# Optimization experiments

Hardware: AMD Instinct MI355X
Metric: run time of the kernel (lower is better)

## Reference

```python
import jax, jax.numpy as jnp
import numpy as np

N = 100000
E = 800000
D_IN = 64
D_HID = 64
D_OUT = 47


def gcn_conv(x, edge_index, W, b):
    # GCNConv with normalize=False: linear transform then sum-aggregate over edges.
    h = x @ W                              # [N, d_out]
    src, dst = edge_index[0], edge_index[1]
    msg = h[src]                           # [E, d_out] gather
    agg = jax.ops.segment_sum(msg, dst, num_segments=N)  # [N, d_out] scatter-add
    return agg + b


def setup_inputs() -> dict:
    key = jax.random.key(0)
    ks = jax.random.split(key, 8)
    x = jax.random.normal(ks[0], (N, D_IN), dtype=jnp.float32)
    edge_index = jax.random.randint(ks[1], (2, E), 0, N, dtype=jnp.int64)
    # Glorot-ish init for weights, zeros for bias (as in GCNConv.reset_parameters)
    def glorot(k, fan_in, fan_out):
        s = jnp.sqrt(6.0 / (fan_in + fan_out))
        return jax.random.uniform(k, (fan_in, fan_out), jnp.float32, -s, s)
    W1 = glorot(ks[2], D_IN, D_HID)
    b1 = jnp.zeros((D_HID,), jnp.float32)
    W2 = glorot(ks[3], D_HID, D_HID)
    b2 = jnp.zeros((D_HID,), jnp.float32)
    W3 = glorot(ks[4], D_HID, D_OUT)
    b3 = jnp.zeros((D_OUT,), jnp.float32)
    return {"x": x, "edge_index": edge_index,
            "W1": W1, "b1": b1, "W2": W2, "b2": b2, "W3": W3, "b3": b3}


def reference(x, edge_index, W1, b1, W2, b2, W3, b3):
    # Layer 1: conv -> relu (dropout is identity at inference)
    h = jax.nn.relu(gcn_conv(x, edge_index, W1, b1))
    # Layer 2
    h = jax.nn.relu(gcn_conv(h, edge_index, W2, b2))
    # Output layer + log_softmax over classes
    out = gcn_conv(h, edge_index, W3, b3)
    return jax.nn.log_softmax(out, axis=-1)
```

## Files before the change

kernel.cpp:

```cpp
#include <hip/hip_runtime.h>
#include <cmath>


#define B1_EPB 4096
#define BKT_SH 8
#define CHUNK  256
#define PSTRIDE 512

typedef __attribute__((ext_vector_type(8))) short bf8;
typedef __attribute__((ext_vector_type(4))) float f4;

__device__ __forceinline__ unsigned int f2bf(float x) {
  unsigned int u = __float_as_uint(x);
  return (u + 0x7FFFu + ((u >> 16) & 1u)) >> 16;
}
__device__ __forceinline__ float bflo(unsigned int u) { return __uint_as_float(u << 16); }
__device__ __forceinline__ float bfhi(unsigned int u) { return __uint_as_float(u & 0xFFFF0000u); }

__global__ void bhist_cvt_k(const int* __restrict__ dsti, int* __restrict__ part,
                            int ne, const float* __restrict__ x,
                            unsigned short* __restrict__ xb, int n4,
                            int nbkt, int nseg) {
  __shared__ int lh[PSTRIDE];
  const int b = blockIdx.x, t = threadIdx.x;
  if (b < nseg) {
    for (int i = t; i < PSTRIDE; i += 256) lh[i] = 0;
    __syncthreads();
    const int base = b * B1_EPB;
    const int m = min(B1_EPB, ne - base);
    for (int i = t; i < m; i += 256) atomicAdd(&lh[dsti[base + i] >> BKT_SH], 1);
    __syncthreads();
    for (int i = t; i < PSTRIDE; i += 256) part[b * PSTRIDE + i] = lh[i];
  }
  const int gid = b * 256 + t, gst = gridDim.x * 256;
  for (int j = gid; j < n4; j += gst) {
    float4 v = ((const float4*)x)[j];
    ushort4 o;
    o.x = (unsigned short)f2bf(v.x); o.y = (unsigned short)f2bf(v.y);
    o.z = (unsigned short)f2bf(v.z); o.w = (unsigned short)f2bf(v.w);
    ((ushort4*)xb)[j] = o;
  }
}

__global__ void bscan_k(const int* __restrict__ part, int* __restrict__ bbase,
                        int* __restrict__ bcur, int nbkt, int nseg, int ne) {
  __shared__ int sh[512];
  const int t = threadIdx.x;
  int s0 = 0, s1 = 0, s2 = 0, s3 = 0, s4 = 0, s5 = 0, s6 = 0, s7 = 0;
  int b = 0;
  for (; b + 7 < nseg; b += 8) {
    s0 += part[(b + 0) * PSTRIDE + t];
    s1 += part[(b + 1) * PSTRIDE + t];
    s2 += part[(b + 2) * PSTRIDE + t];
    s3 += part[(b + 3) * PSTRIDE + t];
    s4 += part[(b + 4) * PSTRIDE + t];
    s5 += part[(b + 5) * PSTRIDE + t];
    s6 += part[(b + 6) * PSTRIDE + t];
    s7 += part[(b + 7) * PSTRIDE + t];
  }
  for (; b < nseg; ++b) s0 += part[b * PSTRIDE + t];
  const int s = ((s0 + s1) + (s2 + s3)) + ((s4 + s5) + (s6 + s7));
  sh[t] = s; __syncthreads();
  for (int o = 1; o < 512; o <<= 1) {
    int v = (t >= o) ? sh[t - o] : 0; __syncthreads();
    sh[t] += v; __syncthreads();
  }
  if (t < nbkt) { int e = sh[t] - s; bbase[t] = e; bcur[t] = e; }
  if (t == 0) bbase[nbkt] = ne;
}

__global__ void bucket_k(const int* __restrict__ srci, const int* __restrict__ dsti,
                         int* __restrict__ bcur, uint2* __restrict__ ebuf,
                         int ne, int nbkt) {
  __shared__ int lhist[512], lbase[512];
  const int t = threadIdx.x;
  const int base = blockIdx.x * B1_EPB;
  const int m = min(B1_EPB, ne - base);
  for (int i = t; i < nbkt; i += 256) lhist[i] = 0;
  __syncthreads();
  for (int i = t; i < m; i += 256) atomicAdd(&lhist[dsti[base + i] >> BKT_SH], 1);
  __syncthreads();
  for (int i = t; i < nbkt; i += 256) {
    int c = lhist[i];
    lbase[i] = c ? atomicAdd(&bcur[i], c) : 0;
  }
  __syncthreads();
  for (int i = t; i < nbkt; i += 256) lhist[i] = 0;
  __syncthreads();
  for (int i = t; i < m; i += 256) {
    const int s = srci[base + i], d = dsti[base + i];
    const int b = d >> BKT_SH;
    const int p = lbase[b] + atomicAdd(&lhist[b], 1);
    ebuf[p] = make_uint2((unsigned)s, (unsigned)d);
  }
}

__global__ void fillb_k(const uint2* __restrict__ ebuf, const int* __restrict__ bbase,
                        int* __restrict__ row_off, int* __restrict__ ssrc,
                        int n, int ne) {
  __shared__ int lcnt[256], lpre[256], lcur[256];
  const int b = blockIdx.x, t = threadIdx.x;
  const int v0 = b << BKT_SH;
  const int nv = min(1 << BKT_SH, n - v0);
  const int start = bbase[b], end = bbase[b + 1];
  lcnt[t] = 0; __syncthreads();
  for (int i = start + t; i < end; i += 256)
    atomicAdd(&lcnt[ebuf[i].y & ((1 << BKT_SH) - 1)], 1);
  __syncthreads();
  const int x = lcnt[t];
  lpre[t] = x; __syncthreads();
  for (int o = 1; o < 256; o <<= 1) {
    int v = (t >= o) ? lpre[t - o] : 0; __syncthreads();
    lpre[t] += v; __syncthreads();
  }
  const int excl = start + lpre[t] - x;
  lcur[t] = excl;
  if (t < nv) row_off[v0 + t] = excl;
  if (t == 0) row_off[v0 + nv] = end;
  __syncthreads();
  for (int i = start + t; i < end; i += 256) {
    const uint2 e = ebuf[i];
    const int p = atomicAdd(&lcur[e.y & ((1 << BKT_SH) - 1)], 1);
    ssrc[p] = (int)e.x;
  }
}

template <int DOUT, bool LS>
__launch_bounds__(256, 4)
__global__ void fused_k(const unsigned short* __restrict__ in,
                        const int* __restrict__ row_off, const int* __restrict__ ssrc,
                        const float* __restrict__ Wm, const float* __restrict__ bin,
                        void* __restrict__ outp, int n) {
  constexpr int NT = (DOUT + 15) / 16;
  const int lane  = threadIdx.x & 63;
  const int wslot = threadIdx.x >> 6;
  const int quad  = lane >> 4;
  const int f16i  = lane & 15;

  __shared__ char rows_raw[4][16 * 144];
  __shared__ int  sidx[4][CHUNK];
  char* my  = rows_raw[wslot];
  int*  sid = sidx[wslot];

  bf8 bfr[2][NT];
#pragma unroll
  for (int s = 0; s < 2; ++s)
#pragma unroll
    for (int t = 0; t < NT; ++t) {
      const int c = t * 16 + f16i;
#pragma unroll
      for (int j = 0; j < 8; ++j) {
        const int k = s * 32 + quad * 8 + j;
        float wv = (c < DOUT) ? Wm[k * DOUT + c] : 0.f;
        bfr[s][t][j] = (short)f2bf(wv);
      }
    }
  float bc[NT];
#pragma unroll
  for (int t = 0; t < NT; ++t) {
    const int c = t * 16 + f16i;
    bc[t] = (c < DOUT) ? bin[c] : 0.f;
  }

  const uint2* in2 = (const uint2*)in;
  const int wid = (int)((blockIdx.x * blockDim.x + threadIdx.x) >> 6);
  const int nwv = (int)((gridDim.x * blockDim.x) >> 6);
  const int ntiles = (n + 15) >> 4;

  for (int tile = wid; tile < ntiles; tile += nwv) {
    const int v0 = tile << 4;
    const int ro_l = row_off[min(v0 + min(lane, 16), n)];
    const int base     = __shfl(ro_l, 0, 64);
    const int tile_end = __shfl(ro_l, 16, 64);
    int ns[4], nE[4];
#pragma unroll
    for (int r = 0; r < 4; ++r) {
      const int m = quad * 4 + r;
      ns[r] = __shfl(ro_l, m, 64);
      nE[r] = __shfl(ro_l, m + 1, 64);
    }

    float4 accA[4], accB[4];
#pragma unroll
    for (int r = 0; r < 4; ++r) {
      accA[r] = make_float4(0.f, 0.f, 0.f, 0.f);
      accB[r] = make_float4(0.f, 0.f, 0.f, 0.f);
    }

    for (int off = base; off < tile_end; off += CHUNK) {
      const int cend = min(tile_end, off + CHUNK);
      const int nL = cend - off;
#pragma unroll
      for (int k = 0; k < CHUNK / 64; ++k) {
        const int p = off + lane + k * 64;
        if (p < cend) sid[lane + k * 64] = ssrc[p];
      }
      asm volatile("s_waitcnt lgkmcnt(0)" ::: "memory");

#pragma unroll
      for (int r = 0; r < 4; ++r) {
        const int ls = max(ns[r], off), le = min(nE[r], cend);
        for (int c = ls; c < le; c += 8) {
          uint2 q[8];
#pragma unroll
          for (int k = 0; k < 8; ++k) {
            const int lofs = min(c - off + k, nL - 1);
            const int s = sid[lofs];
            q[k] = (c + k < le) ? in2[(size_t)s * 16 + f16i]
                                : make_uint2(0u, 0u);
          }
#pragma unroll
          for (int k = 0; k < 8; k += 2) {
            accA[r].x += bflo(q[k].x); accB[r].x += bflo(q[k + 1].x);
            accA[r].y += bfhi(q[k].x); accB[r].y += bfhi(q[k + 1].x);
            accA[r].z += bflo(q[k].y); accB[r].z += bflo(q[k + 1].y);
            accA[r].w += bfhi(q[k].y); accB[r].w += bfhi(q[k + 1].y);
          }
        }
      }
    }

#pragma unroll
    for (int r = 0; r < 4; ++r) {
      const int m = quad * 4 + r;
      uint2 p;
      p.x = f2bf(accA[r].x + accB[r].x) | (f2bf(accA[r].y + accB[r].y) << 16);
      p.y = f2bf(accA[r].z + accB[r].z) | (f2bf(accA[r].w + accB[r].w) << 16);
      *(uint2*)(my + m * 144 + f16i * 8) = p;
    }
    asm volatile("s_waitcnt lgkmcnt(0)" ::: "memory");

    bf8 a0 = *(const bf8*)(my + f16i * 144 + quad * 16);
    bf8 a1 = *(const bf8*)(my + f16i * 144 + quad * 16 + 64);
    f4 acc[NT];
#pragma unroll
    for (int t = 0; t < NT; ++t) {
      f4 z = {0.f, 0.f, 0.f, 0.f};
      acc[t] = __builtin_amdgcn_mfma_f32_16x16x32_bf16(a0, bfr[0][t], z, 0, 0, 0);
      acc[t] = __builtin_amdgcn_mfma_f32_16x16x32_bf16(a1, bfr[1][t], acc[t], 0, 0, 0);
    }

    if (!LS) {
      unsigned short* ob = (unsigned short*)outp;
#pragma unroll
      for (int t = 0; t < NT; ++t)
#pragma unroll
        for (int j = 0; j < 4; ++j) {
          const int v = v0 + quad * 4 + j;
          if (v < n) {
            float val = acc[t][j] + bc[t];
            ob[(size_t)v * 64 + t * 16 + f16i] =
                (unsigned short)f2bf(fmaxf(val, 0.f));
          }
        }
    } else {
      float* ob = (float*)outp;
      float val[NT][4];
#pragma unroll
      for (int t = 0; t < NT; ++t)
#pragma unroll
        for (int j = 0; j < 4; ++j) val[t][j] = acc[t][j] + bc[t];
#pragma unroll
      for (int j = 0; j < 4; ++j) {
        float mx = -INFINITY;
#pragma unroll
        for (int t = 0; t < NT; ++t)
          if (t * 16 + f16i < DOUT) mx = fmaxf(mx, val[t][j]);
#pragma unroll
        for (int o = 1; o <= 8; o <<= 1) mx = fmaxf(mx, __shfl_xor(mx, o, 64));
        float sm = 0.f;
#pragma unroll
        for (int t = 0; t < NT; ++t)
          if (t * 16 + f16i < DOUT) sm += __expf(val[t][j] - mx);
#pragma unroll
        for (int o = 1; o <= 8; o <<= 1) sm += __shfl_xor(sm, o, 64);
        const float lse = mx + __logf(sm);
        const int v = v0 + quad * 4 + j;
        if (v < n) {
#pragma unroll
          for (int t = 0; t < NT; ++t) {
            const int c = t * 16 + f16i;
            if (c < DOUT) ob[(size_t)v * DOUT + c] = val[t][j] - lse;
          }
        }
      }
    }
  }
}

extern "C" void kernel_launch(void* const* d_in, const int* in_sizes, int n_in,
                              void* d_out, int out_size, void* d_ws, size_t ws_size,
                              hipStream_t stream) {
  const float* x  = (const float*)d_in[0];
  const int*   ei = (const int*)d_in[1];
  const float* W1 = (const float*)d_in[2];
  const float* b1 = (const float*)d_in[3];
  const float* W2 = (const float*)d_in[4];
  const float* b2 = (const float*)d_in[5];
  const float* W3 = (const float*)d_in[6];
  const float* b3 = (const float*)d_in[7];
  float* outp = (float*)d_out;

  const int n  = in_sizes[0] / 64;
  const int ne = in_sizes[1] / 2;
  const int* srci = ei;
  const int* dsti = ei + ne;
  const int nbkt = (n + (1 << BKT_SH) - 1) >> BKT_SH;
  const int nseg = (ne + B1_EPB - 1) / B1_EPB;

  const size_t N64 = (size_t)n * 64;
  unsigned short* xb   = (unsigned short*)d_ws;
  unsigned short* bufA = xb + N64;
  unsigned short* bufB = bufA + N64;
  uint2* ebuf   = (uint2*)(bufB + N64);
  int* row_off  = (int*)(ebuf + ne);
  int* part     = row_off + n + 1;
  int* bbase    = part + nseg * PSTRIDE;
  int* bcur     = bbase + nbkt + 1;
  int* ssrc     = bcur + nbkt;

  const int TB = 256;
  const int fus_blocks = 1568;

  bhist_cvt_k<<<784, TB, 0, stream>>>(dsti, part, ne, x, xb, (int)(N64 / 4), nbkt, nseg);
  bscan_k<<<1, 512, 0, stream>>>(part, bbase, bcur, nbkt, nseg, ne);
  bucket_k<<<nseg, TB, 0, stream>>>(srci, dsti, bcur, ebuf, ne, nbkt);
  fillb_k<<<nbkt, TB, 0, stream>>>(ebuf, bbase, row_off, ssrc, n, ne);

  fused_k<64, false><<<fus_blocks, TB, 0, stream>>>(xb,   row_off, ssrc, W1, b1, bufA, n);
  fused_k<64, false><<<fus_blocks, TB, 0, stream>>>(bufA, row_off, ssrc, W2, b2, bufB, n);
  fused_k<47, true ><<<fus_blocks, TB, 0, stream>>>(bufB, row_off, ssrc, W3, b3, outp, n);
}
```

Before: 208.6 us.

## Parallelize bucket totals, reuse per-segment histograms, stage weights in LDS

```diff
diff --git a/kernel.cpp b/kernel.cpp
--- a/kernel.cpp
+++ b/kernel.cpp
@@ -42,24 +42,34 @@
   }
 }
 
-__global__ void bscan_k(const int* __restrict__ part, int* __restrict__ bbase,
-                        int* __restrict__ bcur, int nbkt, int nseg, int ne) {
+__global__ void btot_k(const int* __restrict__ part, int* __restrict__ btot,
+                       int nseg) {
+  __shared__ int sh[256];
+  const int t = threadIdx.x;
+  const int bkt = (blockIdx.x << 6) + (t & 63);
+  int s0 = 0, s1 = 0, s2 = 0, s3 = 0, s4 = 0, s5 = 0, s6 = 0, s7 = 0;
+  int seg = t >> 6;
+  for (; seg + 28 < nseg; seg += 32) {
+    s0 += part[(seg +  0) * PSTRIDE + bkt];
+    s1 += part[(seg +  4) * PSTRIDE + bkt];
+    s2 += part[(seg +  8) * PSTRIDE + bkt];
+    s3 += part[(seg + 12) * PSTRIDE + bkt];
+    s4 += part[(seg + 16) * PSTRIDE + bkt];
+    s5 += part[(seg + 20) * PSTRIDE + bkt];
+    s6 += part[(seg + 24) * PSTRIDE + bkt];
+    s7 += part[(seg + 28) * PSTRIDE + bkt];
+  }
+  for (; seg < nseg; seg += 4) s0 += part[seg * PSTRIDE + bkt];
+  sh[t] = ((s0 + s1) + (s2 + s3)) + ((s4 + s5) + (s6 + s7));
+  __syncthreads();
+  if (t < 64) btot[bkt] = sh[t] + sh[t + 64] + sh[t + 128] + sh[t + 192];
+}
+
+__global__ void bscan_k(const int* __restrict__ btot, int* __restrict__ bbase,
+                        int* __restrict__ bcur, int nbkt, int ne) {
   __shared__ int sh[512];
   const int t = threadIdx.x;
-  int s0 = 0, s1 = 0, s2 = 0, s3 = 0, s4 = 0, s5 = 0, s6 = 0, s7 = 0;
-  int b = 0;
-  for (; b + 7 < nseg; b += 8) {
-    s0 += part[(b + 0) * PSTRIDE + t];
-    s1 += part[(b + 1) * PSTRIDE + t];
-    s2 += part[(b + 2) * PSTRIDE + t];
-    s3 += part[(b + 3) * PSTRIDE + t];
-    s4 += part[(b + 4) * PSTRIDE + t];
-    s5 += part[(b + 5) * PSTRIDE + t];
-    s6 += part[(b + 6) * PSTRIDE + t];
-    s7 += part[(b + 7) * PSTRIDE + t];
-  }
-  for (; b < nseg; ++b) s0 += part[b * PSTRIDE + t];
-  const int s = ((s0 + s1) + (s2 + s3)) + ((s4 + s5) + (s6 + s7));
+  const int s = btot[t];
   sh[t] = s; __syncthreads();
   for (int o = 1; o < 512; o <<= 1) {
     int v = (t >= o) ? sh[t - o] : 0; __syncthreads();
@@ -70,27 +80,22 @@
 }
 
 __global__ void bucket_k(const int* __restrict__ srci, const int* __restrict__ dsti,
-                         int* __restrict__ bcur, uint2* __restrict__ ebuf,
-                         int ne, int nbkt) {
-  __shared__ int lhist[512], lbase[512];
+                         const int* __restrict__ part, int* __restrict__ bcur,
+                         uint2* __restrict__ ebuf, int ne, int nbkt) {
+  __shared__ int lcur[512], lbase[512];
   const int t = threadIdx.x;
   const int base = blockIdx.x * B1_EPB;
   const int m = min(B1_EPB, ne - base);
-  for (int i = t; i < nbkt; i += 256) lhist[i] = 0;
-  __syncthreads();
-  for (int i = t; i < m; i += 256) atomicAdd(&lhist[dsti[base + i] >> BKT_SH], 1);
-  __syncthreads();
   for (int i = t; i < nbkt; i += 256) {
-    int c = lhist[i];
+    const int c = part[blockIdx.x * PSTRIDE + i];
     lbase[i] = c ? atomicAdd(&bcur[i], c) : 0;
-  }
-  __syncthreads();
-  for (int i = t; i < nbkt; i += 256) lhist[i] = 0;
+    lcur[i] = 0;
+  }
   __syncthreads();
   for (int i = t; i < m; i += 256) {
     const int s = srci[base + i], d = dsti[base + i];
     const int b = d >> BKT_SH;
-    const int p = lbase[b] + atomicAdd(&lhist[b], 1);
+    const int p = lbase[b] + atomicAdd(&lcur[b], 1);
     ebuf[p] = make_uint2((unsigned)s, (unsigned)d);
   }
 }
@@ -139,28 +144,26 @@
 
   __shared__ char rows_raw[4][16 * 144];
   __shared__ int  sidx[4][CHUNK];
+  __shared__ unsigned short Wt[64 * 72];
   char* my  = rows_raw[wslot];
   int*  sid = sidx[wslot];
 
-  bf8 bfr[2][NT];
-#pragma unroll
-  for (int s = 0; s < 2; ++s)
-#pragma unroll
-    for (int t = 0; t < NT; ++t) {
-      const int c = t * 16 + f16i;
-#pragma unroll
-      for (int j = 0; j < 8; ++j) {
-        const int k = s * 32 + quad * 8 + j;
-        float wv = (c < DOUT) ? Wm[k * DOUT + c] : 0.f;
-        bfr[s][t][j] = (short)f2bf(wv);
-      }
-    }
+  {
+    const int t = threadIdx.x;
+    for (int i = t; i < 64 * 72; i += 256) Wt[i] = 0;
+    __syncthreads();
+    for (int i = t; i < 64 * DOUT; i += 256) {
+      const int k = i / DOUT, c = i - k * DOUT;
+      Wt[c * 72 + k] = (unsigned short)f2bf(Wm[i]);
+    }
+  }
   float bc[NT];
 #pragma unroll
   for (int t = 0; t < NT; ++t) {
     const int c = t * 16 + f16i;
     bc[t] = (c < DOUT) ? bin[c] : 0.f;
   }
+  __syncthreads();
 
   const uint2* in2 = (const uint2*)in;
   const int wid = (int)((blockIdx.x * blockDim.x + threadIdx.x) >> 6);
@@ -235,9 +238,12 @@
     f4 acc[NT];
 #pragma unroll
     for (int t = 0; t < NT; ++t) {
+      const unsigned short* wp = Wt + (t * 16 + f16i) * 72 + quad * 8;
+      bf8 w0 = *(const bf8*)(wp);
+      bf8 w1 = *(const bf8*)(wp + 32);
       f4 z = {0.f, 0.f, 0.f, 0.f};
-      acc[t] = __builtin_amdgcn_mfma_f32_16x16x32_bf16(a0, bfr[0][t], z, 0, 0, 0);
-      acc[t] = __builtin_amdgcn_mfma_f32_16x16x32_bf16(a1, bfr[1][t], acc[t], 0, 0, 0);
+      acc[t] = __builtin_amdgcn_mfma_f32_16x16x32_bf16(a0, w0, z, 0, 0, 0);
+      acc[t] = __builtin_amdgcn_mfma_f32_16x16x32_bf16(a1, w1, acc[t], 0, 0, 0);
     }
 
     if (!LS) {
@@ -317,14 +323,16 @@
   int* part     = row_off + n + 1;
   int* bbase    = part + nseg * PSTRIDE;
   int* bcur     = bbase + nbkt + 1;
-  int* ssrc     = bcur + nbkt;
+  int* btot     = bcur + nbkt;
+  int* ssrc     = btot + 512;
 
   const int TB = 256;
   const int fus_blocks = 1568;
 
   bhist_cvt_k<<<784, TB, 0, stream>>>(dsti, part, ne, x, xb, (int)(N64 / 4), nbkt, nseg);
-  bscan_k<<<1, 512, 0, stream>>>(part, bbase, bcur, nbkt, nseg, ne);
-  bucket_k<<<nseg, TB, 0, stream>>>(srci, dsti, bcur, ebuf, ne, nbkt);
+  btot_k<<<8, TB, 0, stream>>>(part, btot, nseg);
+  bscan_k<<<1, 512, 0, stream>>>(btot, bbase, bcur, nbkt, ne);
+  bucket_k<<<nseg, TB, 0, stream>>>(srci, dsti, part, bcur, ebuf, ne, nbkt);
   fillb_k<<<nbkt, TB, 0, stream>>>(ebuf, bbase, row_off, ssrc, n, ne);
 
   fused_k<64, false><<<fus_blocks, TB, 0, stream>>>(xb,   row_off, ssrc, W1, b1, bufA, n);
```

Measured after the change: 208.3 us. About the same (-0.2%).
